# Optimization experiments

Hardware: AMD Instinct MI355X
Metric: run time of the kernel (lower is better)

## Reference

```python
import jax, jax.numpy as jnp
import numpy as np

S, D, H, F = 8192, 2048, 2048, 8192
C_GATE = 8.0
EPS = 1e-6


def _rmsnorm(x, w, b):
    # eqx.nn.RMSNorm: x / sqrt(mean(x^2) + eps) * w + b, per row
    inv = jax.lax.rsqrt(jnp.mean(x * x, axis=-1, keepdims=True) + EPS)
    return x * inv * w + b


def _rglru(x, W_in, b_in, W_a, b_a, W_g, b_g, lam, W_out, b_out):
    # Real-Gated LRU (Griffin). x: [S, D] -> [S, D], hidden state size H.
    xh = x @ W_in.T + b_in                      # [S, H]
    r = jax.nn.sigmoid(x @ W_a.T + b_a)         # recurrence gate [S, H]
    g = jax.nn.sigmoid(x @ W_g.T + b_g)         # input gate      [S, H]
    log_a = C_GATE * r * jax.nn.log_sigmoid(lam)  # log a_t, a = sigmoid(lam)^(c*r)
    a = jnp.exp(log_a)                          # [S, H], in (0,1)
    b = jnp.sqrt(1.0 - jnp.exp(2.0 * log_a)) * (g * xh)

    def combine(e1, e2):
        a1, b1 = e1
        a2, b2 = e2
        return (a1 * a2, a2 * b1 + b2)

    _, h = jax.lax.associative_scan(combine, (a, b), axis=0)  # h_t = a_t h_{t-1} + b_t
    return h @ W_out.T + b_out                  # [S, D]


def _ffn(x, w1, b1, w2, b2):
    return jax.nn.gelu(x @ w1.T + b1) @ w2.T + b2


def setup_inputs() -> dict:
    key = jax.random.key(0)
    ks = jax.random.split(key, 16)
    s = 0.02  # weight init scale
    return {
        "x": jax.random.normal(ks[0], (S, D), jnp.float32),
        "W_in": jax.random.normal(ks[1], (H, D), jnp.float32) * s,
        "b_in": jnp.zeros((H,), jnp.float32),
        "W_a": jax.random.normal(ks[2], (H, D), jnp.float32) * s,
        "b_a": jnp.zeros((H,), jnp.float32),
        "W_g": jax.random.normal(ks[3], (H, D), jnp.float32) * s,
        "b_g": jnp.zeros((H,), jnp.float32),
        "lam": jax.random.normal(ks[4], (H,), jnp.float32),
        "W_out": jax.random.normal(ks[5], (D, H), jnp.float32) * s,
        "b_out": jnp.zeros((D,), jnp.float32),
        "ffn_w1": jax.random.normal(ks[6], (F, D), jnp.float32) * s,
        "ffn_b1": jnp.zeros((F,), jnp.float32),
        "ffn_w2": jax.random.normal(ks[7], (D, F), jnp.float32) * s,
        "ffn_b2": jnp.zeros((D,), jnp.float32),
        "act1_w": jax.random.normal(ks[8], (1, D), jnp.float32) * s,
        "act1_b": jnp.zeros((1,), jnp.float32),
        "act2_w": jax.random.normal(ks[9], (1, D), jnp.float32) * s,
        "act2_b": jnp.zeros((1,), jnp.float32),
        "norm1_w": jnp.ones((D,), jnp.float32),
        "norm1_b": jnp.zeros((D,), jnp.float32),
        "norm2_w": jnp.ones((D,), jnp.float32),
        "norm2_b": jnp.zeros((D,), jnp.float32),
        "u1": jax.random.uniform(ks[10], (S, 1), jnp.float32),
        "u2": jax.random.uniform(ks[11], (S, 1), jnp.float32),
    }


def reference(x, W_in, b_in, W_a, b_a, W_g, b_g, lam, W_out, b_out,
              ffn_w1, ffn_b1, ffn_w2, ffn_b2,
              act1_w, act1_b, act2_w, act2_b,
              norm1_w, norm1_b, norm2_w, norm2_b, u1, u2):
    # --- RG-LRU branch (dropout p=0 -> identity) ---
    residual = _rglru(x, W_in, b_in, W_a, b_a, W_g, b_g, lam, W_out, b_out)
    act_prob = jax.nn.sigmoid(residual @ act1_w.T + act1_b)  # [S, 1]
    act = u1 < act_prob                                      # stochastic gate
    residual = jnp.where(act, residual, 0.0)
    x = _rmsnorm(x + residual, norm1_w, norm1_b)
    # --- FFN branch ---
    residual = _ffn(x, ffn_w1, ffn_b1, ffn_w2, ffn_b2)
    act_prob = jax.nn.sigmoid(residual @ act2_w.T + act2_b)
    act = u2 < act_prob
    residual = jnp.where(act, residual, 0.0)
    x = _rmsnorm(x + residual, norm2_w, norm2_b)
    return x
```

## Files before the change

kernel.cpp:

```cpp
#include <hip/hip_runtime.h>

#define LDSW 40
#define SCAN_P 128
#define SCAN_L 64

typedef short short8 __attribute__((ext_vector_type(8)));
typedef float floatx4 __attribute__((ext_vector_type(4)));
typedef unsigned short u16;

__device__ __forceinline__ u16 bf16_rne(float v) {
    unsigned int u = __float_as_uint(v);
    u = u + 0x7fffu + ((u >> 16) & 1u);
    return (u16)(u >> 16);
}
__device__ __forceinline__ float bf16_to_f(u16 h) {
    return __uint_as_float(((unsigned int)h) << 16);
}
__device__ __forceinline__ float sigm(float x) { return 1.f / (1.f + expf(-x)); }
__device__ __forceinline__ float logsig(float x) {
    const float l = log1pf(expf(-fabsf(x)));
    return x >= 0.f ? -l : x - l;
}

__device__ __forceinline__ void cvt8(const float* p, short8& h8, short8& l8) {
    const float4 a = *(const float4*)p;
    const float4 b = *(const float4*)(p + 4);
    const float v[8] = {a.x, a.y, a.z, a.w, b.x, b.y, b.z, b.w};
#pragma unroll
    for (int j = 0; j < 8; ++j) {
        const u16 hh = bf16_rne(v[j]);
        h8[j] = (short)hh;
        l8[j] = (short)bf16_rne(v[j] - bf16_to_f(hh));
    }
}
__device__ __forceinline__ void cvt8h(const float* p, short8& h8) {
    const float4 a = *(const float4*)p;
    const float4 b = *(const float4*)(p + 4);
    const float v[8] = {a.x, a.y, a.z, a.w, b.x, b.y, b.z, b.w};
#pragma unroll
    for (int j = 0; j < 8; ++j) h8[j] = (short)bf16_rne(v[j]);
}

__device__ __forceinline__ void gld16(const u16* g, u16* l) {
    __builtin_amdgcn_global_load_lds(
        (const __attribute__((address_space(1))) void*)g,
        (__attribute__((address_space(3))) void*)l, 16, 0, 0);
}

__device__ __forceinline__ void vmwait8() { asm volatile("s_waitcnt vmcnt(8)" ::: "memory"); }
__device__ __forceinline__ void vmwait4() { asm volatile("s_waitcnt vmcnt(4)" ::: "memory"); }
__device__ __forceinline__ void vmwait0() { asm volatile("s_waitcnt vmcnt(0)" ::: "memory"); }
__device__ __forceinline__ void lgwait0() { asm volatile("s_waitcnt lgkmcnt(0)" ::: "memory"); }
__device__ __forceinline__ void barr()    { asm volatile("s_barrier" ::: "memory"); }

template <int AFMT, int NPROD, int EPI, int ACC, int ST>
__global__ __launch_bounds__(256, 2) void gemm_f32(
    const float* __restrict__ Af, const u16* __restrict__ Au,
    const float* __restrict__ Bf, const float* __restrict__ bias,
    float* C, u16* Chi, u16* Clo, const float* Q,
    long ldA, long ldB, long ldC, int K)
{
    __shared__ __align__(16) u16 sAh[128 * LDSW];
    __shared__ __align__(16) u16 sBh[128 * LDSW];
    __shared__ __align__(16) u16 sAl[NPROD == 3 ? 128 * LDSW : 8];
    __shared__ __align__(16) u16 sBl[NPROD == 3 ? 128 * LDSW : 8];

    const int tid  = threadIdx.x;
    const int lane = tid & 63;
    const int wid  = tid >> 6;
    const int wm   = (wid >> 1) << 6;
    const int wn   = (wid & 1) << 6;
    const int m16  = lane & 15;
    const int kq   = lane >> 4;
    const int koff = kq << 3;
    const long bM  = (long)blockIdx.y << 7;
    const long bN  = (long)blockIdx.x << 7;
    const int sr   = tid >> 2;
    const int sc   = (tid & 3) << 3;

    floatx4 acc[4][4] = {};

#pragma unroll 1
    for (int k0 = 0; k0 < K; k0 += 32) {
        __syncthreads();
#pragma unroll
        for (int i = 0; i < 2; ++i) {
            const int r  = sr + (i << 6);
            const int ls = r * LDSW + sc;
            if constexpr (AFMT == 0) {
                if constexpr (NPROD == 3) {
                    short8 h8, l8;
                    cvt8(Af + (bM + r) * ldA + k0 + sc, h8, l8);
                    *(short8*)&sAh[ls] = h8;
                    *(short8*)&sAl[ls] = l8;
                } else {
                    short8 h8;
                    cvt8h(Af + (bM + r) * ldA + k0 + sc, h8);
                    *(short8*)&sAh[ls] = h8;
                }
            } else {
                *(short8*)&sAh[ls] = *(const short8*)(Au + (bM + r) * ldA + k0 + sc);
            }
            if constexpr (NPROD == 3) {
                short8 h8, l8;
                cvt8(Bf + (bN + r) * ldB + k0 + sc, h8, l8);
                *(short8*)&sBh[ls] = h8;
                *(short8*)&sBl[ls] = l8;
            } else {
                short8 h8;
                cvt8h(Bf + (bN + r) * ldB + k0 + sc, h8);
                *(short8*)&sBh[ls] = h8;
            }
        }
        __syncthreads();

        short8 ah[4], bh[4];
#pragma unroll
        for (int t = 0; t < 4; ++t) {
            ah[t] = *(const short8*)&sAh[(wm + t * 16 + m16) * LDSW + koff];
            bh[t] = *(const short8*)&sBh[(wn + t * 16 + m16) * LDSW + koff];
        }
#pragma unroll
        for (int mi = 0; mi < 4; ++mi)
#pragma unroll
            for (int ni = 0; ni < 4; ++ni)
                acc[mi][ni] = __builtin_amdgcn_mfma_f32_16x16x32_bf16(ah[mi], bh[ni], acc[mi][ni], 0, 0, 0);

        if constexpr (NPROD == 3) {
            short8 al[4], bl[4];
#pragma unroll
            for (int t = 0; t < 4; ++t) {
                al[t] = *(const short8*)&sAl[(wm + t * 16 + m16) * LDSW + koff];
                bl[t] = *(const short8*)&sBl[(wn + t * 16 + m16) * LDSW + koff];
            }
#pragma unroll
            for (int mi = 0; mi < 4; ++mi)
#pragma unroll
                for (int ni = 0; ni < 4; ++ni)
                    acc[mi][ni] = __builtin_amdgcn_mfma_f32_16x16x32_bf16(ah[mi], bl[ni], acc[mi][ni], 0, 0, 0);
#pragma unroll
            for (int mi = 0; mi < 4; ++mi)
#pragma unroll
                for (int ni = 0; ni < 4; ++ni)
                    acc[mi][ni] = __builtin_amdgcn_mfma_f32_16x16x32_bf16(al[mi], bh[ni], acc[mi][ni], 0, 0, 0);
        }
    }

    float bv[4];
#pragma unroll
    for (int ni = 0; ni < 4; ++ni) bv[ni] = bias ? bias[bN + wn + ni * 16 + m16] : 0.f;

#pragma unroll
    for (int mi = 0; mi < 4; ++mi) {
#pragma unroll
        for (int ni = 0; ni < 4; ++ni) {
#pragma unroll
            for (int r = 0; r < 4; ++r) {
                const long grow = bM + wm + mi * 16 + (kq << 2) + r;
                const long gcol = bN + wn + ni * 16 + m16;
                const long idx  = grow * ldC + gcol;
                float v = acc[mi][ni][r] + bv[ni];
                if constexpr (ACC) v += C[idx];
                if constexpr (EPI == 1) v *= Q[idx];
                if constexpr (EPI == 2)
                    v = 0.5f * v * (1.f + tanhf(0.7978845608028654f * (v + 0.044715f * v * v * v)));
                if constexpr (ST == 1) {
                    const u16 h = bf16_rne(v);
                    Chi[idx] = h;
                    Clo[idx] = bf16_rne(v - bf16_to_f(h));
                } else {
                    C[idx] = v;
                }
            }
        }
    }
}

template <int NPROD, int BFMT, int EPI, int ACC, int ST, int DOT>
__global__ __launch_bounds__(256, 2) void gemm_sp(
    const u16* __restrict__ Ah, const u16* __restrict__ Al,
    const u16* __restrict__ Bh, const u16* __restrict__ Bl,
    const float* __restrict__ Bf, const float* __restrict__ bias,
    float* C, u16* Chi, const float* Q,
    const float* __restrict__ vvec, float* dacc,
    long ldA, long ldB, long ldC, int K)
{
    __shared__ __align__(16) u16 sAh[128 * 32];
    __shared__ __align__(16) u16 sBh[128 * 32];
    __shared__ __align__(16) u16 sAl[NPROD == 3 ? 128 * 32 : 8];
    __shared__ __align__(16) u16 sBl[NPROD == 3 ? 128 * 32 : 8];

    const int tid  = threadIdx.x;
    const int lane = tid & 63;
    const int wid  = tid >> 6;
    const int wm   = (wid >> 1) << 6;
    const int wn   = (wid & 1) << 6;
    const int m16  = lane & 15;
    const int kq   = lane >> 4;
    const long bM  = (long)blockIdx.y << 7;
    const long bN  = (long)blockIdx.x << 7;

    const int  drow = (wid << 5) + (lane >> 2);
    const int  qsrc = (((lane & 3) ^ ((lane >> 3) & 3)) << 3);
    const long a0   = (bM + drow) * ldA + qsrc;
    const long a1   = a0 + 16 * ldA;
    const long b0   = (bN + drow) * ldB + qsrc;
    const long b1   = b0 + 16 * ldB;
    u16* const lA0  = &sAh[(wid << 5) << 5];
    u16* const lA1  = lA0 + 512;
    u16* const lB0  = &sBh[(wid << 5) << 5];
    u16* const lB1  = lB0 + 512;
    u16* const lAl0 = &sAl[NPROD == 3 ? ((wid << 5) << 5) : 0];
    u16* const lAl1 = lAl0 + (NPROD == 3 ? 512 : 0);
    u16* const lBl0 = &sBl[NPROD == 3 ? ((wid << 5) << 5) : 0];
    u16* const lBl1 = lBl0 + (NPROD == 3 ? 512 : 0);

    const int sr  = tid >> 2;
    const int sc  = (tid & 3) << 3;
    const int wch = (((tid & 3) ^ ((sr >> 1) & 3)) << 3);

    const int kr = ((kq ^ ((m16 >> 1) & 3)) << 3);

    floatx4 acc[4][4] = {};

#pragma unroll 1
    for (int k0 = 0; k0 < K; k0 += 32) {
        __syncthreads();
        gld16(Ah + a0 + k0, lA0);
        gld16(Ah + a1 + k0, lA1);
        if constexpr (NPROD == 3) {
            gld16(Al + a0 + k0, lAl0);
            gld16(Al + a1 + k0, lAl1);
        }
        if constexpr (BFMT == 1) {
            gld16(Bh + b0 + k0, lB0);
            gld16(Bh + b1 + k0, lB1);
            if constexpr (NPROD == 3) {
                gld16(Bl + b0 + k0, lBl0);
                gld16(Bl + b1 + k0, lBl1);
            }
        } else {
#pragma unroll
            for (int i = 0; i < 2; ++i) {
                const int r = sr + (i << 6);
                short8 h8, l8;
                cvt8(Bf + (bN + r) * ldB + k0 + sc, h8, l8);
                *(short8*)&sBh[(r << 5) + wch] = h8;
                *(short8*)&sBl[(r << 5) + wch] = l8;
            }
        }
        __syncthreads();

        short8 ah[4], bh[4];
#pragma unroll
        for (int t = 0; t < 4; ++t) {
            ah[t] = *(const short8*)&sAh[((wm + t * 16 + m16) << 5) + kr];
            bh[t] = *(const short8*)&sBh[((wn + t * 16 + m16) << 5) + kr];
        }
#pragma unroll
        for (int mi = 0; mi < 4; ++mi)
#pragma unroll
            for (int ni = 0; ni < 4; ++ni)
                acc[mi][ni] = __builtin_amdgcn_mfma_f32_16x16x32_bf16(ah[mi], bh[ni], acc[mi][ni], 0, 0, 0);

        if constexpr (NPROD == 3) {
            short8 al[4], bl[4];
#pragma unroll
            for (int t = 0; t < 4; ++t) {
                al[t] = *(const short8*)&sAl[((wm + t * 16 + m16) << 5) + kr];
                bl[t] = *(const short8*)&sBl[((wn + t * 16 + m16) << 5) + kr];
            }
#pragma unroll
            for (int mi = 0; mi < 4; ++mi)
#pragma unroll
                for (int ni = 0; ni < 4; ++ni)
                    acc[mi][ni] = __builtin_amdgcn_mfma_f32_16x16x32_bf16(ah[mi], bl[ni], acc[mi][ni], 0, 0, 0);
#pragma unroll
            for (int mi = 0; mi < 4; ++mi)
#pragma unroll
                for (int ni = 0; ni < 4; ++ni)
                    acc[mi][ni] = __builtin_amdgcn_mfma_f32_16x16x32_bf16(al[mi], bh[ni], acc[mi][ni], 0, 0, 0);
        }
    }

    float bv[4];
#pragma unroll
    for (int ni = 0; ni < 4; ++ni) bv[ni] = bias ? bias[bN + wn + ni * 16 + m16] : 0.f;
    float vv[4] = {}, ls[4] = {};
    if constexpr (EPI == 3 || DOT == 1) {
#pragma unroll
        for (int ni = 0; ni < 4; ++ni) {
            vv[ni] = vvec[bN + wn + ni * 16 + m16];
            if constexpr (EPI == 3) ls[ni] = logsig(vv[ni]);
        }
    }
    float ds[4][4] = {};

#pragma unroll
    for (int mi = 0; mi < 4; ++mi) {
#pragma unroll
        for (int ni = 0; ni < 4; ++ni) {
#pragma unroll
            for (int r = 0; r < 4; ++r) {
                const long grow = bM + wm + mi * 16 + (kq << 2) + r;
                const long gcol = bN + wn + ni * 16 + m16;
                const long idx  = grow * ldC + gcol;
                float v = acc[mi][ni][r] + bv[ni];
                if constexpr (EPI == 1) v *= Q[idx];
                if constexpr (EPI == 2)
                    v = 0.5f * v * (1.f + tanhf(0.7978845608028654f * (v + 0.044715f * v * v * v)));
                if constexpr (EPI == 3) v = expf(8.f * sigm(v) * ls[ni]);
                if constexpr (EPI == 4) {
                    const float a = Q[idx];
                    v = sqrtf(fmaxf(1.f - a * a, 0.f)) * sigm(v);
                }
                if constexpr (ACC) v += C[idx];
                if constexpr (DOT) ds[mi][r] += v * vv[ni];
                if constexpr (ST == 1) Chi[idx] = bf16_rne(v);
                else C[idx] = v;
            }
        }
    }

    if constexpr (DOT) {
#pragma unroll
        for (int mi = 0; mi < 4; ++mi)
#pragma unroll
            for (int r = 0; r < 4; ++r) {
                float s = ds[mi][r];
                s += __shfl_xor(s, 1);
                s += __shfl_xor(s, 2);
                s += __shfl_xor(s, 4);
                s += __shfl_xor(s, 8);
                if (m16 == 0)
                    atomicAdd(&dacc[bM + wm + mi * 16 + (kq << 2) + r], s);
            }
    }
}

template <int NPROD, int EPI, int ACC, int ST, int DOT>
__global__ __launch_bounds__(512, 2) void gemm8v2(
    const u16* __restrict__ Ah, const u16* __restrict__ Al,
    const u16* __restrict__ Bh, const u16* __restrict__ Bl,
    const float* __restrict__ bias,
    float* C, u16* Chi, const float* __restrict__ Q,
    const float* __restrict__ vvec, float* dacc,
    long ldA, long ldB, long ldC, int K)
{
    constexpr int NPL = (NPROD == 3) ? 4 : 2;
    __shared__ __align__(16) u16 lds[2][NPL][8192];

    const int tid  = threadIdx.x;
    const int lane = tid & 63;
    const int wid  = tid >> 6;
    const int wr   = wid >> 2;
    const int wc   = wid & 3;
    const int m16  = lane & 15;
    const int kq   = lane >> 4;
    const int bst  = wid & 3;

    const int nbx = gridDim.x;
    const int lin = blockIdx.y * nbx + blockIdx.x;
    const int nwg = nbx * gridDim.y;
    int bx = blockIdx.x, by = blockIdx.y;
    if ((nwg & 7) == 0) {
        const int s = (lin & 7) * (nwg >> 3) + (lin >> 3);
        bx = s % nbx;
        by = s / nbx;
    }
    const long bM = (long)by << 8;
    const long bN = (long)bx << 8;

    const int  drow = (wid << 5) + (lane >> 2);
    const int  qsrc = (((lane & 3) ^ ((lane >> 3) & 3)) << 3);
    const u16* gA0  = Ah + (bM + drow) * ldA + qsrc;
    const u16* gA1  = gA0 + (ldA << 4);
    const u16* gB0  = Bh + (bN + drow) * ldB + qsrc;
    const u16* gB1  = gB0 + (ldB << 4);
    const u16* gAl0 = (NPROD == 3 ? Al : Ah) + (bM + drow) * ldA + qsrc;
    const u16* gAl1 = gAl0 + (ldA << 4);
    const u16* gBl0 = (NPROD == 3 ? Bl : Bh) + (bN + drow) * ldB + qsrc;
    const u16* gBl1 = gBl0 + (ldB << 4);

    const int lwb = wid << 10;
    const int kr  = ((kq ^ ((m16 >> 1) & 3)) << 3);
    const int NT  = K >> 5;

    auto stageA = [&](int buf, int t) {
        const long k0 = (long)t << 5;
        gld16(gA0 + k0, &lds[buf][0][lwb]);
        gld16(gA1 + k0, &lds[buf][0][lwb + 512]);
        if constexpr (NPROD == 3) {
            gld16(gAl0 + k0, &lds[buf][2][lwb]);
            gld16(gAl1 + k0, &lds[buf][2][lwb + 512]);
        }
    };
    auto stageB = [&](int buf, int t) {
        const long k0 = (long)t << 5;
        gld16(gB0 + k0, &lds[buf][1][lwb]);
        gld16(gB1 + k0, &lds[buf][1][lwb + 512]);
        if constexpr (NPROD == 3) {
            gld16(gBl0 + k0, &lds[buf][3][lwb]);
            gld16(gBl1 + k0, &lds[buf][3][lwb + 512]);
        }
    };

    floatx4 acc[8][4] = {};
    short8 bhr[4], blr[4];
    short8 fa[2][4];

    stageA(0, 0); stageB(0, 0);
    stageA(1, 1); stageB(1, 1);
    if constexpr (NPROD == 3) vmwait8(); else vmwait4();
    barr();

    const int arow = (wr << 7) + m16;
    const int brow = (wc << 6) + m16;

#pragma unroll 1
    for (int t = 0; t < NT; ++t) {
        const int p  = t & 1;
        const bool pf = (t + 2 < NT);

#pragma unroll
        for (int ni = 0; ni < 4; ++ni) {
            const int rb = (brow + (ni << 4)) << 5;
            bhr[ni] = *(const short8*)&lds[p][1][rb + kr];
            if constexpr (NPROD == 3) blr[ni] = *(const short8*)&lds[p][3][rb + kr];
        }
        fa[0][0] = *(const short8*)&lds[p][0][(arow << 5) + kr];
        fa[0][1] = *(const short8*)&lds[p][0][((arow + 16) << 5) + kr];
        if constexpr (NPROD == 3) {
            fa[0][2] = *(const short8*)&lds[p][2][(arow << 5) + kr];
            fa[0][3] = *(const short8*)&lds[p][2][((arow + 16) << 5) + kr];
        }

#pragma unroll
        for (int q = 0; q < 4; ++q) {
            const int cur = q & 1;
            const int nxt = cur ^ 1;
            if (q < 3) {
                const int r0 = arow + ((q + 1) << 5);
                fa[nxt][0] = *(const short8*)&lds[p][0][(r0 << 5) + kr];
                fa[nxt][1] = *(const short8*)&lds[p][0][((r0 + 16) << 5) + kr];
                if constexpr (NPROD == 3) {
                    fa[nxt][2] = *(const short8*)&lds[p][2][(r0 << 5) + kr];
                    fa[nxt][3] = *(const short8*)&lds[p][2][((r0 + 16) << 5) + kr];
                }
            }
            if (pf) {
                if (q == 1) stageB(p, t + 2);
                if (q == (bst >= 2 ? 3 : bst + 1)) stageA(p, t + 2);
            }
            __builtin_amdgcn_s_setprio(1);
#pragma unroll
            for (int ni = 0; ni < 4; ++ni) {
                acc[2 * q][ni]     = __builtin_amdgcn_mfma_f32_16x16x32_bf16(fa[cur][0], bhr[ni], acc[2 * q][ni], 0, 0, 0);
                acc[2 * q + 1][ni] = __builtin_amdgcn_mfma_f32_16x16x32_bf16(fa[cur][1], bhr[ni], acc[2 * q + 1][ni], 0, 0, 0);
            }
            if constexpr (NPROD == 3) {
#pragma unroll
                for (int ni = 0; ni < 4; ++ni) {
                    acc[2 * q][ni]     = __builtin_amdgcn_mfma_f32_16x16x32_bf16(fa[cur][0], blr[ni], acc[2 * q][ni], 0, 0, 0);
                    acc[2 * q + 1][ni] = __builtin_amdgcn_mfma_f32_16x16x32_bf16(fa[cur][1], blr[ni], acc[2 * q + 1][ni], 0, 0, 0);
                }
#pragma unroll
                for (int ni = 0; ni < 4; ++ni) {
                    acc[2 * q][ni]     = __builtin_amdgcn_mfma_f32_16x16x32_bf16(fa[cur][2], bhr[ni], acc[2 * q][ni], 0, 0, 0);
                    acc[2 * q + 1][ni] = __builtin_amdgcn_mfma_f32_16x16x32_bf16(fa[cur][3], bhr[ni], acc[2 * q + 1][ni], 0, 0, 0);
                }
            }
            __builtin_amdgcn_s_setprio(0);
            lgwait0();
            if (q == 3) {
                if (pf) { if constexpr (NPROD == 3) vmwait8(); else vmwait4(); }
                else vmwait0();
            }
            barr();
        }
    }

    float bv[4];
#pragma unroll
    for (int ni = 0; ni < 4; ++ni) bv[ni] = bias ? bias[bN + (wc << 6) + (ni << 4) + m16] : 0.f;
    float vv[4] = {}, ls[4] = {};
    if constexpr (EPI == 3 || DOT == 1) {
#pragma unroll
        for (int ni = 0; ni < 4; ++ni) {
            vv[ni] = vvec[bN + (wc << 6) + (ni << 4) + m16];
            if constexpr (EPI == 3) ls[ni] = logsig(vv[ni]);
        }
    }
    float ds[8][4] = {};

#pragma unroll
    for (int mi = 0; mi < 8; ++mi) {
#pragma unroll
        for (int ni = 0; ni < 4; ++ni) {
#pragma unroll
            for (int r = 0; r < 4; ++r) {
                const long grow = bM + (wr << 7) + (mi << 4) + (kq << 2) + r;
                const long gcol = bN + (wc << 6) + (ni << 4) + m16;
                const long idx  = grow * ldC + gcol;
                float v = acc[mi][ni][r] + bv[ni];
                if constexpr (EPI == 1) v *= Q[idx];
                if constexpr (EPI == 2)
                    v = 0.5f * v * (1.f + tanhf(0.7978845608028654f * (v + 0.044715f * v * v * v)));
                if constexpr (EPI == 3) v = expf(8.f * sigm(v) * ls[ni]);
                if constexpr (EPI == 4) {
                    const float a = Q[idx];
                    v = sqrtf(fmaxf(1.f - a * a, 0.f)) * sigm(v);
                }
                if constexpr (ACC) v += C[idx];
                if constexpr (DOT) ds[mi][r] += v * vv[ni];
                if constexpr (ST == 1) Chi[idx] = bf16_rne(v);
                else C[idx] = v;
            }
        }
    }

    if constexpr (DOT) {
#pragma unroll
        for (int mi = 0; mi < 8; ++mi)
#pragma unroll
            for (int r = 0; r < 4; ++r) {
                float s = ds[mi][r];
                s += __shfl_xor(s, 1);
                s += __shfl_xor(s, 2);
                s += __shfl_xor(s, 4);
                s += __shfl_xor(s, 8);
                if (m16 == 0)
                    atomicAdd(&dacc[bM + (wr << 7) + (mi << 4) + (kq << 2) + r], s);
            }
    }
}

template <int HASLO>
__global__ __launch_bounds__(256) void split_kernel(
    const float* __restrict__ src, long lds,
    u16* __restrict__ hi, u16* __restrict__ lo, long ldd)
{
    const long r = blockIdx.x;
    const int  c = threadIdx.x << 3;
    const float* p = src + r * lds + c;
    const float4 a = *(const float4*)p;
    const float4 b = *(const float4*)(p + 4);
    const float v[8] = {a.x, a.y, a.z, a.w, b.x, b.y, b.z, b.w};
    short8 h8, l8;
#pragma unroll
    for (int j = 0; j < 8; ++j) {
        const u16 hh = bf16_rne(v[j]);
        h8[j] = (short)hh;
        if constexpr (HASLO) l8[j] = (short)bf16_rne(v[j] - bf16_to_f(hh));
    }
    *(short8*)&hi[r * ldd + c] = h8;
    if constexpr (HASLO) *(short8*)&lo[r * ldd + c] = l8;
}

__global__ __launch_bounds__(256) void zb2init_kernel(
    float* __restrict__ zb2, const float* __restrict__ zc2)
{
    zb2[blockIdx.x * 256 + threadIdx.x] = zc2[0];
}

__global__ __launch_bounds__(256) void aq_kernel(
    float* za, float* zg, const float* __restrict__ lam)
{
    const long i = ((long)blockIdx.x * 256 + threadIdx.x) * 4;
    const int  c = (int)(i & 2047);
    const float4 zav = *(const float4*)(za + i);
    const float4 zgv = *(const float4*)(zg + i);
    const float4 lmv = *(const float4*)(lam + c);
    float4 av, qv;
    const float zaa[4] = {zav.x, zav.y, zav.z, zav.w};
    const float zga[4] = {zgv.x, zgv.y, zgv.z, zgv.w};
    const float lma[4] = {lmv.x, lmv.y, lmv.z, lmv.w};
    float aa[4], qa[4];
#pragma unroll
    for (int j = 0; j < 4; ++j) {
        const float r  = sigm(zaa[j]);
        const float g  = sigm(zga[j]);
        const float la = 8.f * r * logsig(lma[j]);
        aa[j] = expf(la);
        qa[j] = sqrtf(fmaxf(1.f - expf(2.f * la), 0.f)) * g;
    }
    av.x = aa[0]; av.y = aa[1]; av.z = aa[2]; av.w = aa[3];
    qv.x = qa[0]; qv.y = qa[1]; qv.z = qa[2]; qv.w = qa[3];
    *(float4*)(za + i) = av;
    *(float4*)(zg + i) = qv;
}

__global__ __launch_bounds__(256) void scan_partial(
    const float* __restrict__ A, const float* __restrict__ B,
    float* __restrict__ Aagg, float* __restrict__ Bagg)
{
    const int c = blockIdx.x * 256 + threadIdx.x;
    const int p = blockIdx.y;
    const long base = (long)p * SCAN_L * 2048 + c;
    float Ar = 1.f, Br = 0.f;
    for (int t = 0; t < SCAN_L; ++t) {
        const float at = A[base + (long)t * 2048];
        const float bt = B[base + (long)t * 2048];
        Ar *= at;
        Br = Br * at + bt;
    }
    Aagg[p * 2048 + c] = Ar;
    Bagg[p * 2048 + c] = Br;
}

__global__ __launch_bounds__(256) void scan_combine(
    const float* __restrict__ Aagg, const float* __restrict__ Bagg,
    float* __restrict__ Hini)
{
    const int c = blockIdx.x * 256 + threadIdx.x;
    float h = 0.f;
    for (int p = 0; p < SCAN_P; ++p) {
        Hini[p * 2048 + c] = h;
        h = Aagg[p * 2048 + c] * h + Bagg[p * 2048 + c];
    }
}

__global__ __launch_bounds__(256) void scan_final(
    float* A, const float* __restrict__ B, const float* __restrict__ Hini,
    u16* __restrict__ Hhi)
{
    const int c = blockIdx.x * 256 + threadIdx.x;
    const int p = blockIdx.y;
    const long base = (long)p * SCAN_L * 2048 + c;
    float h = Hini[p * 2048 + c];
    for (int t = 0; t < SCAN_L; ++t) {
        const long idx = base + (long)t * 2048;
        h = A[idx] * h + B[idx];
        A[idx] = h;
        if (Hhi) Hhi[idx] = bf16_rne(h);
    }
}

__global__ __launch_bounds__(256) void vpart_kernel(
    const float* __restrict__ W, const float* __restrict__ w,
    float* __restrict__ part, long ldW, int dchunk)
{
    const int j  = blockIdx.x * 256 + threadIdx.x;
    const int d0 = blockIdx.y * dchunk;
    float s = 0.f;
    for (int d = 0; d < dchunk; ++d) s += W[(long)(d0 + d) * ldW + j] * w[d0 + d];
    part[(long)blockIdx.y * ldW + j] = s;
}

__global__ __launch_bounds__(256) void vreduce_kernel(
    const float* __restrict__ part, float* __restrict__ v, long ldW, int nch)
{
    const int j = blockIdx.x * 256 + threadIdx.x;
    float s = 0.f;
    for (int c = 0; c < nch; ++c) s += part[(long)c * ldW + j];
    v[j] = s;
}

__global__ __launch_bounds__(256) void dotc_kernel(
    const float* __restrict__ a, const float* __restrict__ b,
    const float* __restrict__ bias1, float* __restrict__ out)
{
    __shared__ float red[4];
    const int tid = threadIdx.x, lane = tid & 63, wid = tid >> 6;
    float s = 0.f;
    for (int d = tid; d < 2048; d += 256) s += a[d] * b[d];
#pragma unroll
    for (int off = 32; off > 0; off >>= 1) s += __shfl_down(s, off);
    if (lane == 0) red[wid] = s;
    __syncthreads();
    if (tid == 0) out[0] = red[0] + red[1] + red[2] + red[3] + bias1[0];
}

template <int INIT>
__global__ __launch_bounds__(256) void zacc_kernel(
    const u16* __restrict__ uHi, const u16* __restrict__ uLo,
    const float* __restrict__ v2s, const float* __restrict__ zc,
    float* __restrict__ zb, int L)
{
    __shared__ float red[4];
    const int tid = threadIdx.x, lane = tid & 63, wid = tid >> 6;
    const long s = blockIdx.x;
    const long base = s * (long)L;
    float dot = 0.f;
    for (int f = tid; f < L; f += 256)
        dot += (bf16_to_f(uHi[base + f]) + bf16_to_f(uLo[base + f])) * v2s[f];
#pragma unroll
    for (int off = 32; off > 0; off >>= 1) dot += __shfl_down(dot, off);
    if (lane == 0) red[wid] = dot;
    __syncthreads();
    if (tid == 0) {
        const float t = red[0] + red[1] + red[2] + red[3];
        zb[s] = INIT ? (zc[0] + t) : (zb[s] + t);
    }
}

__global__ __launch_bounds__(256) void gate1_kernel(
    const float* __restrict__ x, float* res1x1,
    const float* __restrict__ h,
    const float* __restrict__ v1, const float* __restrict__ zc1,
    const float* __restrict__ u1,
    const float* __restrict__ nw, const float* __restrict__ nb)
{
    __shared__ float red[4];
    const int tid = threadIdx.x, lane = tid & 63, wid = tid >> 6;
    const long s = blockIdx.x;
    const long base = s * 2048;

    float dot = 0.f;
#pragma unroll
    for (int k = 0; k < 8; ++k) {
        const int d = tid + (k << 8);
        dot += h[base + d] * v1[d];
    }
#pragma unroll
    for (int off = 32; off > 0; off >>= 1) dot += __shfl_down(dot, off);
    if (lane == 0) red[wid] = dot;
    __syncthreads();
    const float z = red[0] + red[1] + red[2] + red[3] + zc1[0];
    __syncthreads();

    const float g = (u1[s] < sigm(z)) ? 1.f : 0.f;

    float yv[8];
    float ss = 0.f;
#pragma unroll
    for (int k = 0; k < 8; ++k) {
        const int d = tid + (k << 8);
        const float y = x[base + d] + g * res1x1[base + d];
        yv[k] = y;
        ss += y * y;
    }
#pragma unroll
    for (int off = 32; off > 0; off >>= 1) ss += __shfl_down(ss, off);
    if (lane == 0) red[wid] = ss;
    __syncthreads();
    const float inv = rsqrtf((red[0] + red[1] + red[2] + red[3]) * (1.f / 2048.f) + 1e-6f);

#pragma unroll
    for (int k = 0; k < 8; ++k) {
        const int d = tid + (k << 8);
        res1x1[base + d] = yv[k] * inv * nw[d] + nb[d];
    }
}

__global__ __launch_bounds__(256) void gate1s_kernel(
    const float* __restrict__ x, float* res1x1,
    const float* __restrict__ h,
    const float* __restrict__ v1, const float* __restrict__ zc1,
    const float* __restrict__ u1,
    const float* __restrict__ nw, const float* __restrict__ nb)
{
    __shared__ float red[4];
    const int tid = threadIdx.x, lane = tid & 63, wid = tid >> 6;
    const long s = blockIdx.x;
    const long base = s * 2048;

    float dot = 0.f;
#pragma unroll
    for (int k = 0; k < 8; ++k) {
        const int d = tid + (k << 8);
        dot += h[base + d] * v1[d];
    }
#pragma unroll
    for (int off = 32; off > 0; off >>= 1) dot += __shfl_down(dot, off);
    if (lane == 0) red[wid] = dot;
    __syncthreads();
    const float z = red[0] + red[1] + red[2] + red[3] + zc1[0];
    __syncthreads();

    const float g = (u1[s] < sigm(z)) ? 1.f : 0.f;

    float yv[8];
    float ss = 0.f;
#pragma unroll
    for (int k = 0; k < 8; ++k) {
        const int d = tid + (k << 8);
        const float y = x[base + d] + g * res1x1[base + d];
        yv[k] = y;
        ss += y * y;
    }
#pragma unroll
    for (int off = 32; off > 0; off >>= 1) ss += __shfl_down(ss, off);
    if (lane == 0) red[wid] = ss;
    __syncthreads();
    const float inv = rsqrtf((red[0] + red[1] + red[2] + red[3]) * (1.f / 2048.f) + 1e-6f);

    u16* xs = (u16*)res1x1;
    const long sb = s * 4096;
#pragma unroll
    for (int k = 0; k < 8; ++k) {
        const int d = tid + (k << 8);
        const float o = yv[k] * inv * nw[d] + nb[d];
        const u16 hh = bf16_rne(o);
        xs[sb + d] = hh;
        xs[sb + 2048 + d] = bf16_rne(o - bf16_to_f(hh));
    }
}

__global__ __launch_bounds__(256) void gate2_kernel(
    float* x1out, const float* __restrict__ res2,
    const float* __restrict__ zb2, const float* __restrict__ u2,
    const float* __restrict__ nw, const float* __restrict__ nb)
{
    __shared__ float red[4];
    const int tid = threadIdx.x, lane = tid & 63, wid = tid >> 6;
    const long s = blockIdx.x;
    const long base = s * 2048;

    const float g = (u2[s] < sigm(zb2[s])) ? 1.f : 0.f;

    float yv[8];
    float ss = 0.f;
#pragma unroll
    for (int k = 0; k < 8; ++k) {
        const int d = tid + (k << 8);
        const float y = x1out[base + d] + g * res2[base + d];
        yv[k] = y;
        ss += y * y;
    }
#pragma unroll
    for (int off = 32; off > 0; off >>= 1) ss += __shfl_down(ss, off);
    if (lane == 0) red[wid] = ss;
    __syncthreads();
    const float inv = rsqrtf((red[0] + red[1] + red[2] + red[3]) * (1.f / 2048.f) + 1e-6f);

#pragma unroll
    for (int k = 0; k < 8; ++k) {
        const int d = tid + (k << 8);
        x1out[base + d] = yv[k] * inv * nw[d] + nb[d];
    }
}

__global__ __launch_bounds__(256) void gate2s_kernel(
    float* x1out, const float* __restrict__ res2,
    const float* __restrict__ zb2, const float* __restrict__ u2,
    const float* __restrict__ nw, const float* __restrict__ nb)
{
    __shared__ float red[4];
    const int tid = threadIdx.x, lane = tid & 63, wid = tid >> 6;
    const long s = blockIdx.x;
    const long base = s * 2048;
    const u16* xs = (const u16*)x1out;
    const long sb = s * 4096;

    const float g = (u2[s] < sigm(zb2[s])) ? 1.f : 0.f;

    float yv[8];
    float ss = 0.f;
#pragma unroll
    for (int k = 0; k < 8; ++k) {
        const int d = tid + (k << 8);
        const float x1 = bf16_to_f(xs[sb + d]) + bf16_to_f(xs[sb + 2048 + d]);
        const float y = x1 + g * res2[base + d];
        yv[k] = y;
        ss += y * y;
    }
#pragma unroll
    for (int off = 32; off > 0; off >>= 1) ss += __shfl_down(ss, off);
    if (lane == 0) red[wid] = ss;
    __syncthreads();
    const float inv = rsqrtf((red[0] + red[1] + red[2] + red[3]) * (1.f / 2048.f) + 1e-6f);

#pragma unroll
    for (int k = 0; k < 8; ++k) {
        const int d = tid + (k << 8);
        x1out[base + d] = yv[k] * inv * nw[d] + nb[d];
    }
}

extern "C" void kernel_launch(void* const* d_in, const int* in_sizes, int n_in,
                              void* d_out, int out_size, void* d_ws, size_t ws_size,
                              hipStream_t stream)
{
    const float* x     = (const float*)d_in[0];
    const float* W_in  = (const float*)d_in[1];
    const float* b_in  = (const float*)d_in[2];
    const float* W_a   = (const float*)d_in[3];
    const float* b_a   = (const float*)d_in[4];
    const float* W_g   = (const float*)d_in[5];
    const float* b_g   = (const float*)d_in[6];
    const float* lam   = (const float*)d_in[7];
    const float* W_out = (const float*)d_in[8];
    const float* b_out = (const float*)d_in[9];
    const float* w1    = (const float*)d_in[10];
    const float* fb1   = (const float*)d_in[11];
    const float* w2    = (const float*)d_in[12];
    const float* fb2   = (const float*)d_in[13];
    const float* a1w   = (const float*)d_in[14];
    const float* a1b   = (const float*)d_in[15];
    const float* a2w   = (const float*)d_in[16];
    const float* a2b   = (const float*)d_in[17];
    const float* n1w   = (const float*)d_in[18];
    const float* n1b   = (const float*)d_in[19];
    const float* n2w   = (const float*)d_in[20];
    const float* n2b   = (const float*)d_in[21];
    const float* u1    = (const float*)d_in[22];
    const float* u2    = (const float*)d_in[23];
    (void)in_sizes; (void)n_in; (void)out_size;

    float* dob = (float*)d_out;

    char* ws = (char*)d_ws;
    size_t o = 0;
    auto take = [&](size_t bytes) -> char* {
        char* p = ws + o;
        o += (bytes + 255) & ~(size_t)255;
        return p;
    };

    float* Aagg = (float*)take((size_t)SCAN_P * 2048 * 4);
    float* Bagg = (float*)take((size_t)SCAN_P * 2048 * 4);
    float* Hini = (float*)take((size_t)SCAN_P * 2048 * 4);
    float* v1   = (float*)take(2048 * 4);
    float* v2   = (float*)take(8192 * 4);
    float* vp   = (float*)take(16 * 8192 * 4);
    float* zc1  = (float*)take(256);
    float* zc2  = (float*)take(256);
    float* zb2  = (float*)take(8192 * 4);

    float* slabA = (float*)take(64ull << 20);
    const bool pathA = ws_size >= o + (64ull << 20);
    float* slabB = nullptr;
    float* res2b = nullptr;
    float* slabW = nullptr;
    if (pathA) {
        slabB = (float*)take(64ull << 20);
        if (ws_size >= o + (16ull << 20)) slabW = (float*)take(16ull << 20);
    } else {
        res2b = (float*)take(16ull << 20);
    }
    if (o > ws_size) return;

    const dim3 blk(256);
    const dim3 blk8(512);
    const dim3 g8(8, 32);

    vpart_kernel<<<dim3(8, 16), blk, 0, stream>>>(W_out, a1w, vp, 2048, 128);
    vreduce_kernel<<<8, blk, 0, stream>>>(vp, v1, 2048, 16);
    vpart_kernel<<<dim3(32, 16), blk, 0, stream>>>(w2, a2w, vp, 8192, 128);
    vreduce_kernel<<<32, blk, 0, stream>>>(vp, v2, 8192, 16);
    dotc_kernel<<<1, blk, 0, stream>>>(b_out, a1w, a1b, zc1);
    dotc_kernel<<<1, blk, 0, stream>>>(fb2, a2w, a2b, zc2);

    if (pathA) {
        u16* const xh = (u16*)slabA;
        u16* const xl = xh + (1u << 24);
        split_kernel<1><<<8192, blk, 0, stream>>>(x, 2048, xh, xl, 2048);

        if (slabW) {
            u16* const wH = (u16*)slabW;
            u16* const wL = wH + (1u << 22);
            split_kernel<1><<<2048, blk, 0, stream>>>(W_a, 2048, wH, wL, 2048);
            gemm8v2<3, 3, 0, 0, 0><<<g8, blk8, 0, stream>>>(
                xh, xl, wH, wL, b_a, slabB, nullptr, nullptr, lam, nullptr,
                2048, 2048, 2048, 2048);
            split_kernel<1><<<2048, blk, 0, stream>>>(W_g, 2048, wH, wL, 2048);
            gemm8v2<3, 4, 0, 0, 0><<<g8, blk8, 0, stream>>>(
                xh, xl, wH, wL, b_g, dob, nullptr, slabB, nullptr, nullptr,
                2048, 2048, 2048, 2048);
            split_kernel<1><<<2048, blk, 0, stream>>>(W_in, 2048, wH, wL, 2048);
            gemm8v2<3, 1, 0, 0, 0><<<g8, blk8, 0, stream>>>(
                xh, xl, wH, wL, b_in, dob, nullptr, dob, nullptr, nullptr,
                2048, 2048, 2048, 2048);
        } else {
            gemm_sp<3, 0, 3, 0, 0, 0><<<dim3(16, 64), blk, 0, stream>>>(
                xh, xl, nullptr, nullptr, W_a, b_a, slabB, nullptr, nullptr, lam, nullptr,
                2048, 2048, 2048, 2048);
            gemm_sp<3, 0, 4, 0, 0, 0><<<dim3(16, 64), blk, 0, stream>>>(
                xh, xl, nullptr, nullptr, W_g, b_g, dob, nullptr, slabB, nullptr, nullptr,
                2048, 2048, 2048, 2048);
            gemm_sp<3, 0, 1, 0, 0, 0><<<dim3(16, 64), blk, 0, stream>>>(
                xh, xl, nullptr, nullptr, W_in, b_in, dob, nullptr, dob, nullptr, nullptr,
                2048, 2048, 2048, 2048);
        }

        u16* const hH = (u16*)slabA;
        scan_partial<<<dim3(8, SCAN_P), blk, 0, stream>>>(slabB, dob, Aagg, Bagg);
        scan_combine<<<8, blk, 0, stream>>>(Aagg, Bagg, Hini);
        scan_final<<<dim3(8, SCAN_P), blk, 0, stream>>>(slabB, dob, Hini, hH);

        u16* const woH = hH + (1u << 24);
        split_kernel<0><<<2048, blk, 0, stream>>>(W_out, 2048, woH, nullptr, 2048);
        gemm8v2<1, 0, 0, 0, 0><<<g8, blk8, 0, stream>>>(
            hH, nullptr, woH, nullptr, b_out, dob, nullptr, nullptr, nullptr, nullptr,
            2048, 2048, 2048, 2048);

        gate1s_kernel<<<8192, blk, 0, stream>>>(x, dob, slabB, v1, zc1, u1, n1w, n1b);

        zb2init_kernel<<<32, blk, 0, stream>>>(zb2, zc2);

        u16* const uH  = (u16*)slabA;
        u16* const w1H = uH + (1u << 24);
        u16* const w1L = w1H + (1u << 22);
        u16* const w2H = w1H + (1u << 23);
        u16* const x1h = (u16*)dob;
        for (int c = 0; c < 4; ++c) {
            const long f0 = (long)c << 11;
            split_kernel<1><<<2048, blk, 0, stream>>>(w1 + f0 * 2048, 2048, w1H, w1L, 2048);
            split_kernel<0><<<2048, blk, 0, stream>>>(w2 + f0, 8192, w2H, nullptr, 2048);
            gemm8v2<3, 2, 0, 1, 1><<<g8, blk8, 0, stream>>>(
                x1h, x1h + 2048, w1H, w1L, fb1 + f0, nullptr, uH, nullptr,
                v2 + f0, zb2, 4096, 2048, 2048, 2048);
            if (c == 0)
                gemm8v2<1, 0, 0, 0, 0><<<g8, blk8, 0, stream>>>(
                    uH, nullptr, w2H, nullptr, fb2, slabB, nullptr, nullptr, nullptr, nullptr,
                    2048, 2048, 2048, 2048);
            else
                gemm8v2<1, 0, 1, 0, 0><<<g8, blk8, 0, stream>>>(
                    uH, nullptr, w2H, nullptr, nullptr, slabB, nullptr, nullptr, nullptr, nullptr,
                    2048, 2048, 2048, 2048);
        }
        gate2s_kernel<<<8192, blk, 0, stream>>>(dob, slabB, zb2, u2, n2w, n2b);
    } else {
        u16* uHi = (u16*)slabA;
        u16* uLo = uHi + (1u << 24);

        gemm_f32<0, 3, 0, 0, 0><<<dim3(16, 64), blk, 0, stream>>>(
            x, nullptr, W_a, b_a, slabA, nullptr, nullptr, nullptr, 2048, 2048, 2048, 2048);
        gemm_f32<0, 3, 0, 0, 0><<<dim3(16, 64), blk, 0, stream>>>(
            x, nullptr, W_g, b_g, dob, nullptr, nullptr, nullptr, 2048, 2048, 2048, 2048);
        aq_kernel<<<16384, blk, 0, stream>>>(slabA, dob, lam);
        gemm_f32<0, 3, 1, 0, 0><<<dim3(16, 64), blk, 0, stream>>>(
            x, nullptr, W_in, b_in, dob, nullptr, nullptr, dob, 2048, 2048, 2048, 2048);
        scan_partial<<<dim3(8, SCAN_P), blk, 0, stream>>>(slabA, dob, Aagg, Bagg);
        scan_combine<<<8, blk, 0, stream>>>(Aagg, Bagg, Hini);
        scan_final<<<dim3(8, SCAN_P), blk, 0, stream>>>(slabA, dob, Hini, nullptr);
        gemm_f32<0, 1, 0, 0, 0><<<dim3(16, 64), blk, 0, stream>>>(
            slabA, nullptr, W_out, b_out, dob, nullptr, nullptr, nullptr, 2048, 2048, 2048, 2048);
        gate1_kernel<<<8192, blk, 0, stream>>>(x, dob, slabA, v1, zc1, u1, n1w, n1b);
        for (int rb = 0; rb < 4; ++rb) {
            const long roff = (long)rb * 2048;
            gemm_f32<0, 3, 2, 0, 1><<<dim3(64, 16), blk, 0, stream>>>(
                dob + roff * 2048, nullptr, w1, fb1,
                nullptr, uHi, uLo, nullptr, 2048, 2048, 8192, 2048);
            zacc_kernel<1><<<2048, blk, 0, stream>>>(uHi, uLo, v2, zc2, zb2 + roff, 8192);
            gemm_f32<1, 1, 0, 0, 0><<<dim3(16, 16), blk, 0, stream>>>(
                nullptr, uHi, w2, fb2, res2b, nullptr, nullptr, nullptr,
                8192, 8192, 2048, 8192);
            gate2_kernel<<<2048, blk, 0, stream>>>(
                dob + roff * 2048, res2b, zb2 + roff, u2 + roff, n2w, n2b);
        }
    }
}
```

Before: 2.216 ms.

## Simplify GEMM main loop to single-barrier staging after compute

Replaces the interleaved per-quarter A/B prefetch and four barriers per k-step with a single load of all A and B tiles issued after the MFMA block finishes. A fragments are loaded inline instead of being double-buffered in registers. This cuts the barrier count and register pressure, but the global-to-LDS loads no longer overlap with the MFMAs of the same iteration, since the kernel waits on them right after issuing.

After: 2.279 ms. 1.03x slower.

```diff
diff --git a/kernel.cpp b/kernel.cpp
--- a/kernel.cpp
+++ b/kernel.cpp
@@ -357,7 +357,6 @@
     const int wc   = wid & 3;
     const int m16  = lane & 15;
     const int kq   = lane >> 4;
-    const int bst  = wid & 3;
 
     const int nbx = gridDim.x;
     const int lin = blockIdx.y * nbx + blockIdx.x;
@@ -386,31 +385,24 @@
     const int kr  = ((kq ^ ((m16 >> 1) & 3)) << 3);
     const int NT  = K >> 5;
 
-    auto stageA = [&](int buf, int t) {
+    auto stage = [&](int buf, int t) {
         const long k0 = (long)t << 5;
         gld16(gA0 + k0, &lds[buf][0][lwb]);
         gld16(gA1 + k0, &lds[buf][0][lwb + 512]);
+        gld16(gB0 + k0, &lds[buf][1][lwb]);
+        gld16(gB1 + k0, &lds[buf][1][lwb + 512]);
         if constexpr (NPROD == 3) {
             gld16(gAl0 + k0, &lds[buf][2][lwb]);
             gld16(gAl1 + k0, &lds[buf][2][lwb + 512]);
-        }
-    };
-    auto stageB = [&](int buf, int t) {
-        const long k0 = (long)t << 5;
-        gld16(gB0 + k0, &lds[buf][1][lwb]);
-        gld16(gB1 + k0, &lds[buf][1][lwb + 512]);
-        if constexpr (NPROD == 3) {
             gld16(gBl0 + k0, &lds[buf][3][lwb]);
             gld16(gBl1 + k0, &lds[buf][3][lwb + 512]);
         }
     };
 
     floatx4 acc[8][4] = {};
-    short8 bhr[4], blr[4];
-    short8 fa[2][4];
-
-    stageA(0, 0); stageB(0, 0);
-    stageA(1, 1); stageB(1, 1);
+
+    stage(0, 0);
+    stage(1, 1);
     if constexpr (NPROD == 3) vmwait8(); else vmwait4();
     barr();
 
@@ -419,65 +411,53 @@
 
 #pragma unroll 1
     for (int t = 0; t < NT; ++t) {
-        const int p  = t & 1;
-        const bool pf = (t + 2 < NT);
-
+        const int p = t & 1;
+
+        short8 bh[4], bl[4];
 #pragma unroll
         for (int ni = 0; ni < 4; ++ni) {
             const int rb = (brow + (ni << 4)) << 5;
-            bhr[ni] = *(const short8*)&lds[p][1][rb + kr];
-            if constexpr (NPROD == 3) blr[ni] = *(const short8*)&lds[p][3][rb + kr];
-        }
-        fa[0][0] = *(const short8*)&lds[p][0][(arow << 5) + kr];
-        fa[0][1] = *(const short8*)&lds[p][0][((arow + 16) << 5) + kr];
-        if constexpr (NPROD == 3) {
-            fa[0][2] = *(const short8*)&lds[p][2][(arow << 5) + kr];
-            fa[0][3] = *(const short8*)&lds[p][2][((arow + 16) << 5) + kr];
-        }
-
-#pragma unroll
-        for (int q = 0; q < 4; ++q) {
-            const int cur = q & 1;
-            const int nxt = cur ^ 1;
-            if (q < 3) {
-                const int r0 = arow + ((q + 1) << 5);
-                fa[nxt][0] = *(const short8*)&lds[p][0][(r0 << 5) + kr];
-                fa[nxt][1] = *(const short8*)&lds[p][0][((r0 + 16) << 5) + kr];
-                if constexpr (NPROD == 3) {
-                    fa[nxt][2] = *(const short8*)&lds[p][2][(r0 << 5) + kr];
-                    fa[nxt][3] = *(const short8*)&lds[p][2][((r0 + 16) << 5) + kr];
+            bh[ni] = *(const short8*)&lds[p][1][rb + kr];
+            if constexpr (NPROD == 3) bl[ni] = *(const short8*)&lds[p][3][rb + kr];
+        }
+        __builtin_amdgcn_s_setprio(1);
+#pragma unroll
+        for (int s = 0; s < 4; ++s) {
+            const int r0 = arow + (s << 5);
+            const short8 ah0 = *(const short8*)&lds[p][0][(r0 << 5) + kr];
+            const short8 ah1 = *(const short8*)&lds[p][0][((r0 + 16) << 5) + kr];
+#pragma unroll
+            for (int ni = 0; ni < 4; ++ni) {
+                acc[2 * s][ni]     = __builtin_amdgcn_mfma_f32_16x16x32_bf16(ah0, bh[ni], acc[2 * s][ni], 0, 0, 0);
+                acc[2 * s + 1][ni] = __builtin_amdgcn_mfma_f32_16x16x32_bf16(ah1, bh[ni], acc[2 * s + 1][ni], 0, 0, 0);
+            }
+            if constexpr (NPROD == 3) {
+                const short8 al0 = *(const short8*)&lds[p][2][(r0 << 5) + kr];
+                const short8 al1 = *(const short8*)&lds[p][2][((r0 + 16) << 5) + kr];
+#pragma unroll
+                for (int ni = 0; ni < 4; ++ni) {
+                    acc[2 * s][ni]     = __builtin_amdgcn_mfma_f32_16x16x32_bf16(ah0, bl[ni], acc[2 * s][ni], 0, 0, 0);
+                    acc[2 * s + 1][ni] = __builtin_amdgcn_mfma_f32_16x16x32_bf16(ah1, bl[ni], acc[2 * s + 1][ni], 0, 0, 0);
                 }
-            }
-            if (pf) {
-                if (q == 1) stageB(p, t + 2);
-                if (q == (bst >= 2 ? 3 : bst + 1)) stageA(p, t + 2);
-            }
-            __builtin_amdgcn_s_setprio(1);
-#pragma unroll
-            for (int ni = 0; ni < 4; ++ni) {
-                acc[2 * q][ni]     = __builtin_amdgcn_mfma_f32_16x16x32_bf16(fa[cur][0], bhr[ni], acc[2 * q][ni], 0, 0, 0);
-                acc[2 * q + 1][ni] = __builtin_amdgcn_mfma_f32_16x16x32_bf16(fa[cur][1], bhr[ni], acc[2 * q + 1][ni], 0, 0, 0);
-            }
-            if constexpr (NPROD == 3) {
 #pragma unroll
                 for (int ni = 0; ni < 4; ++ni) {
-                    acc[2 * q][ni]     = __builtin_amdgcn_mfma_f32_16x16x32_bf16(fa[cur][0], blr[ni], acc[2 * q][ni], 0, 0, 0);
-                    acc[2 * q + 1][ni] = __builtin_amdgcn_mfma_f32_16x16x32_bf16(fa[cur][1], blr[ni], acc[2 * q + 1][ni], 0, 0, 0);
+                    acc[2 * s][ni]     = __builtin_amdgcn_mfma_f32_16x16x32_bf16(al0, bh[ni], acc[2 * s][ni], 0, 0, 0);
+                    acc[2 * s + 1][ni] = __builtin_amdgcn_mfma_f32_16x16x32_bf16(al1, bh[ni], acc[2 * s + 1][ni], 0, 0, 0);
                 }
-#pragma unroll
-                for (int ni = 0; ni < 4; ++ni) {
-                    acc[2 * q][ni]     = __builtin_amdgcn_mfma_f32_16x16x32_bf16(fa[cur][2], bhr[ni], acc[2 * q][ni], 0, 0, 0);
-                    acc[2 * q + 1][ni] = __builtin_amdgcn_mfma_f32_16x16x32_bf16(fa[cur][3], bhr[ni], acc[2 * q + 1][ni], 0, 0, 0);
-                }
-            }
-            __builtin_amdgcn_s_setprio(0);
-            lgwait0();
-            if (q == 3) {
-                if (pf) { if constexpr (NPROD == 3) vmwait8(); else vmwait4(); }
-                else vmwait0();
-            }
-            barr();
-        }
+            }
+        }
+        __builtin_amdgcn_s_setprio(0);
+
+        lgwait0();
+        barr();
+
+        if (t + 2 < NT) {
+            stage(p, t + 2);
+            if constexpr (NPROD == 3) vmwait8(); else vmwait4();
+        } else {
+            vmwait0();
+        }
+        barr();
     }
 
     float bv[4];
```

## Add 128x128 single-pass bf16 GEMM for W_out/W2 and fuse FFN weight splits

Applied to the files above, without the earlier changes.

Introduces a new 128x128-tile, 256-thread MFMA GEMM kernel with double-buffered LDS staging, XOR-swizzled loads and grouped block remapping. It replaces the larger 512-thread gemm8v2 kernel for the single-precision-pass W_out and FFN W2 GEMMs. The w1 and w2 bf16 split kernels inside the FFN loop are also merged into one launch. The aim is better occupancy and L2 locality for the plain bf16 GEMMs and one fewer launch per chunk. The trade-off is a smaller tile, which means more global loads per FLOP.

After: 2.469 ms. 11.4% more time.

```diff
diff --git a/kernel.cpp b/kernel.cpp
--- a/kernel.cpp
+++ b/kernel.cpp
@@ -535,6 +535,113 @@
     }
 }
 
+template <int ACC>
+__global__ __launch_bounds__(256, 4) void gemm41(
+    const u16* __restrict__ Ah, const u16* __restrict__ Bh,
+    const float* __restrict__ bias, float* C,
+    long ldA, long ldB, long ldC, int K)
+{
+    __shared__ __align__(16) u16 lds[2][2][4096];
+
+    const int tid  = threadIdx.x;
+    const int lane = tid & 63;
+    const int wid  = tid >> 6;
+    const int wr   = wid >> 1;
+    const int wc   = wid & 1;
+    const int m16  = lane & 15;
+    const int kq   = lane >> 4;
+
+    const int nbx = gridDim.x;
+    const int lin = blockIdx.y * nbx + blockIdx.x;
+    const int nwg = nbx * gridDim.y;
+    int bx = blockIdx.x, by = blockIdx.y;
+    if ((nwg & 7) == 0) {
+        const int s = (lin & 7) * (nwg >> 3) + (lin >> 3);
+        bx = s % nbx;
+        by = s / nbx;
+    }
+    const long bM = (long)by << 7;
+    const long bN = (long)bx << 7;
+
+    const int  drow = (wid << 5) + (lane >> 2);
+    const int  qsrc = (((lane & 3) ^ ((lane >> 3) & 3)) << 3);
+    const u16* gA0  = Ah + (bM + drow) * ldA + qsrc;
+    const u16* gA1  = gA0 + (ldA << 4);
+    const u16* gB0  = Bh + (bN + drow) * ldB + qsrc;
+    const u16* gB1  = gB0 + (ldB << 4);
+
+    const int lwb = wid << 10;
+    const int kr  = ((kq ^ ((m16 >> 1) & 3)) << 3);
+    const int NT  = K >> 5;
+
+    auto stage = [&](int buf, int t) {
+        const long k0 = (long)t << 5;
+        gld16(gA0 + k0, &lds[buf][0][lwb]);
+        gld16(gA1 + k0, &lds[buf][0][lwb + 512]);
+        gld16(gB0 + k0, &lds[buf][1][lwb]);
+        gld16(gB1 + k0, &lds[buf][1][lwb + 512]);
+    };
+
+    floatx4 acc[4][4] = {};
+
+    stage(0, 0);
+    stage(1, 1);
+    vmwait4();
+    barr();
+
+    const int arow = (wr << 6) + m16;
+    const int brow = (wc << 6) + m16;
+
+#pragma unroll 1
+    for (int t = 0; t < NT; ++t) {
+        const int p = t & 1;
+
+        short8 bh[4];
+#pragma unroll
+        for (int ni = 0; ni < 4; ++ni)
+            bh[ni] = *(const short8*)&lds[p][1][((brow + (ni << 4)) << 5) + kr];
+        __builtin_amdgcn_s_setprio(1);
+#pragma unroll
+        for (int mi = 0; mi < 4; ++mi) {
+            const short8 ah = *(const short8*)&lds[p][0][((arow + (mi << 4)) << 5) + kr];
+#pragma unroll
+            for (int ni = 0; ni < 4; ++ni)
+                acc[mi][ni] = __builtin_amdgcn_mfma_f32_16x16x32_bf16(ah, bh[ni], acc[mi][ni], 0, 0, 0);
+        }
+        __builtin_amdgcn_s_setprio(0);
+
+        lgwait0();
+        barr();
+        if (t + 2 < NT) {
+            stage(p, t + 2);
+            vmwait4();
+        } else {
+            vmwait0();
+        }
+        barr();
+    }
+
+    float bv[4];
+#pragma unroll
+    for (int ni = 0; ni < 4; ++ni) bv[ni] = bias ? bias[bN + (wc << 6) + (ni << 4) + m16] : 0.f;
+
+#pragma unroll
+    for (int mi = 0; mi < 4; ++mi) {
+#pragma unroll
+        for (int ni = 0; ni < 4; ++ni) {
+#pragma unroll
+            for (int r = 0; r < 4; ++r) {
+                const long grow = bM + (wr << 6) + (mi << 4) + (kq << 2) + r;
+                const long gcol = bN + (wc << 6) + (ni << 4) + m16;
+                const long idx  = grow * ldC + gcol;
+                float v = acc[mi][ni][r] + bv[ni];
+                if constexpr (ACC) v += C[idx];
+                C[idx] = v;
+            }
+        }
+    }
+}
+
 template <int HASLO>
 __global__ __launch_bounds__(256) void split_kernel(
     const float* __restrict__ src, long lds,
@@ -555,6 +662,39 @@
     }
     *(short8*)&hi[r * ldd + c] = h8;
     if constexpr (HASLO) *(short8*)&lo[r * ldd + c] = l8;
+}
+
+__global__ __launch_bounds__(256) void splitw3_kernel(
+    const float* __restrict__ w1c, const float* __restrict__ w2c, long ldw2,
+    u16* __restrict__ w1H, u16* __restrict__ w1L, u16* __restrict__ w2H)
+{
+    const long r = blockIdx.x;
+    const int  c = threadIdx.x << 3;
+    {
+        const float* p = w1c + r * 2048 + c;
+        const float4 a = *(const float4*)p;
+        const float4 b = *(const float4*)(p + 4);
+        const float v[8] = {a.x, a.y, a.z, a.w, b.x, b.y, b.z, b.w};
+        short8 h8, l8;
+#pragma unroll
+        for (int j = 0; j < 8; ++j) {
+            const u16 hh = bf16_rne(v[j]);
+            h8[j] = (short)hh;
+            l8[j] = (short)bf16_rne(v[j] - bf16_to_f(hh));
+        }
+        *(short8*)&w1H[r * 2048 + c] = h8;
+        *(short8*)&w1L[r * 2048 + c] = l8;
+    }
+    {
+        const float* p = w2c + r * ldw2 + c;
+        const float4 a = *(const float4*)p;
+        const float4 b = *(const float4*)(p + 4);
+        const float v[8] = {a.x, a.y, a.z, a.w, b.x, b.y, b.z, b.w};
+        short8 h8;
+#pragma unroll
+        for (int j = 0; j < 8; ++j) h8[j] = (short)bf16_rne(v[j]);
+        *(short8*)&w2H[r * 2048 + c] = h8;
+    }
 }
 
 __global__ __launch_bounds__(256) void zb2init_kernel(
@@ -934,6 +1074,7 @@
     const dim3 blk(256);
     const dim3 blk8(512);
     const dim3 g8(8, 32);
+    const dim3 g41(16, 64);
 
     vpart_kernel<<<dim3(8, 16), blk, 0, stream>>>(W_out, a1w, vp, 2048, 128);
     vreduce_kernel<<<8, blk, 0, stream>>>(vp, v1, 2048, 16);
@@ -981,9 +1122,8 @@
 
         u16* const woH = hH + (1u << 24);
         split_kernel<0><<<2048, blk, 0, stream>>>(W_out, 2048, woH, nullptr, 2048);
-        gemm8v2<1, 0, 0, 0, 0><<<g8, blk8, 0, stream>>>(
-            hH, nullptr, woH, nullptr, b_out, dob, nullptr, nullptr, nullptr, nullptr,
-            2048, 2048, 2048, 2048);
+        gemm41<0><<<g41, blk, 0, stream>>>(
+            hH, woH, b_out, dob, 2048, 2048, 2048, 2048);
 
         gate1s_kernel<<<8192, blk, 0, stream>>>(x, dob, slabB, v1, zc1, u1, n1w, n1b);
 
@@ -996,19 +1136,17 @@
         u16* const x1h = (u16*)dob;
         for (int c = 0; c < 4; ++c) {
             const long f0 = (long)c << 11;
-            split_kernel<1><<<2048, blk, 0, stream>>>(w1 + f0 * 2048, 2048, w1H, w1L, 2048);
-            split_kernel<0><<<2048, blk, 0, stream>>>(w2 + f0, 8192, w2H, nullptr, 2048);
+            splitw3_kernel<<<2048, blk, 0, stream>>>(
+                w1 + f0 * 2048, w2 + f0, 8192, w1H, w1L, w2H);
             gemm8v2<3, 2, 0, 1, 1><<<g8, blk8, 0, stream>>>(
                 x1h, x1h + 2048, w1H, w1L, fb1 + f0, nullptr, uH, nullptr,
                 v2 + f0, zb2, 4096, 2048, 2048, 2048);
             if (c == 0)
-                gemm8v2<1, 0, 0, 0, 0><<<g8, blk8, 0, stream>>>(
-                    uH, nullptr, w2H, nullptr, fb2, slabB, nullptr, nullptr, nullptr, nullptr,
-                    2048, 2048, 2048, 2048);
+                gemm41<0><<<g41, blk, 0, stream>>>(
+                    uH, w2H, fb2, slabB, 2048, 2048, 2048, 2048);
             else
-                gemm8v2<1, 0, 1, 0, 0><<<g8, blk8, 0, stream>>>(
-                    uH, nullptr, w2H, nullptr, nullptr, slabB, nullptr, nullptr, nullptr, nullptr,
-                    2048, 2048, 2048, 2048);
+                gemm41<1><<<g41, blk, 0, stream>>>(
+                    uH, w2H, nullptr, slabB, 2048, 2048, 2048, 2048);
         }
         gate2s_kernel<<<8192, blk, 0, stream>>>(dob, slabB, zb2, u2, n2w, n2b);
     } else {
```
